# Performance work log

Measured on AMD Instinct MI355X. Metric: run time of the kernel, lower is better.

## Reference

```python
import jax, jax.numpy as jnp
import numpy as np

EPS = 1e-6


def _mlp(x, Ws, bs):
    # 5-layer MLP, exact (erf) GELU between layers, matching torch.nn.GELU()
    for W, b in zip(Ws[:-1], bs[:-1]):
        x = jax.nn.gelu(x @ W + b, approximate=False)
    return x @ Ws[-1] + bs[-1]


def setup_inputs() -> dict:
    key = jax.random.key(0)
    ks = jax.random.split(key, 16)
    B, H, D, NT = 262144, 256, 128, 16
    # deformation gradient near identity -> det(F) > 0 so log(det) is finite
    F = jnp.eye(3, dtype=jnp.float32)[None] + 0.05 * jax.random.normal(ks[0], (B, 3, 3), dtype=jnp.float32)
    C = 0.1 * jax.random.normal(ks[1], (B, 3, 3), dtype=jnp.float32)
    emb = 0.02 * jax.random.normal(ks[2], (NT, D), dtype=jnp.float32)
    dims = [16 + 9 + D, H, H, H, H, 9]
    inp = {"F": F, "C": C, "emb": emb, "traj_ids": 3}
    for i in range(5):
        inp[f"W{i+1}"] = jax.random.normal(ks[3 + 2 * i], (dims[i], dims[i + 1]), dtype=jnp.float32) / np.sqrt(dims[i]).astype(np.float32)
        inp[f"b{i+1}"] = jnp.zeros((dims[i + 1],), dtype=jnp.float32)
    return inp


def reference(F, C, emb, traj_ids, W1, b1, W2, b2, W3, b3, W4, b4, W5, b5):
    B = F.shape[0]
    U, sigma, Vh = jnp.linalg.svd(F)          # batched 3x3 SVD
    R = U @ Vh                                 # polar rotation, == torch U @ V^T
    Ft = jnp.swapaxes(F, -1, -2)
    FtF = Ft @ F
    det = jnp.linalg.det(F)
    f00 = jnp.maximum(F[:, 0, 0], EPS)
    # normalize_input=True branch: subtract 1 from each invariant
    I1 = sigma - 1.0                                   # [B,3]
    I2 = (FtF - jnp.eye(3, dtype=F.dtype)).reshape(B, 9)
    I3 = det[:, None] - 1.0
    I4 = jnp.log(det)[:, None] - 1.0
    I5 = f00[:, None] - 1.0
    I6 = jnp.log(f00)[:, None] - 1.0
    strain = jnp.concatenate([I1, I2, I3, I4, I5, I6], axis=1)  # [B,16]
    latent = jnp.broadcast_to(emb[traj_ids][None, :], (B, emb.shape[1]))
    feats = jnp.concatenate([strain, C.reshape(B, 9), latent], axis=-1)
    out = _mlp(feats, [W1, W2, W3, W4, W5], [b1, b2, b3, b4, b5])  # [B,9]
    x = out.reshape(B, 3, 3)
    x = 0.5 * (jnp.swapaxes(x, -1, -2) + x)    # symmetrize
    P = R @ x
    cauchy = P @ Ft
    return cauchy
```

## Files before the change

kernel.cpp:

```cpp
#include <hip/hip_runtime.h>

typedef _Float16 f16;
typedef _Float16 f16x8 __attribute__((ext_vector_type(8)));
typedef float f32x2 __attribute__((ext_vector_type(2)));
typedef float f32x4 __attribute__((ext_vector_type(4)));
typedef float f32x16 __attribute__((ext_vector_type(16)));

#define MROWS 128
#define THREADS 512
#define HSTR 264

#define WS_B1EFF 0
#define WS_W1H   1024
#define WS_W2H   (WS_W1H + 16384)
#define WS_W3H   (WS_W2H + 131072)
#define WS_W4H   (WS_W3H + 131072)
#define WS_W5H   (WS_W4H + 131072)
#define WS_END   (WS_W5H + 8192)

__global__ void prep_kernel(const float* __restrict__ emb, const int* __restrict__ traj,
                            const float* __restrict__ W1, const float* __restrict__ b1,
                            const float* __restrict__ W2, const float* __restrict__ W3,
                            const float* __restrict__ W4, const float* __restrict__ W5,
                            float* __restrict__ b1eff,
                            f16* __restrict__ W1h, f16* __restrict__ W2h,
                            f16* __restrict__ W3h, f16* __restrict__ W4h,
                            f16* __restrict__ W5h) {
  if (blockIdx.x == 816) {
    __shared__ float lat[128];
    int t = *traj;
    if (threadIdx.x < 128) lat[threadIdx.x] = emb[t * 128 + threadIdx.x];
    __syncthreads();
    int n = threadIdx.x;
    float s0 = 0.f, s1 = 0.f, s2 = 0.f, s3 = 0.f;
#pragma unroll 4
    for (int d = 0; d < 128; d += 4) {
      s0 = fmaf(lat[d + 0], W1[(25 + d) * 256 + n], s0);
      s1 = fmaf(lat[d + 1], W1[(26 + d) * 256 + n], s1);
      s2 = fmaf(lat[d + 2], W1[(27 + d) * 256 + n], s2);
      s3 = fmaf(lat[d + 3], W1[(28 + d) * 256 + n], s3);
    }
    b1eff[n] = b1[n] + ((s0 + s1) + (s2 + s3));
    return;
  }
  int i = blockIdx.x * 256 + threadIdx.x;
  if (i < 8192) {
    int n = i >> 5, k = i & 31;
    W1h[i] = (f16)((k < 25) ? W1[k * 256 + n] : 0.0f);
  } else if (i < 73728) {
    int j = i - 8192; int k = j >> 8, n = j & 255;
    W2h[n * 256 + k] = (f16)W2[j];
  } else if (i < 139264) {
    int j = i - 73728; int k = j >> 8, n = j & 255;
    W3h[n * 256 + k] = (f16)W3[j];
  } else if (i < 204800) {
    int j = i - 139264; int k = j >> 8, n = j & 255;
    W4h[n * 256 + k] = (f16)W4[j];
  } else if (i < 208896) {
    int j = i - 204800; int n = j >> 8, k = j & 255;
    W5h[j] = (f16)((n < 9) ? W5[k * 9 + n] : 0.0f);
  }
}

__device__ __forceinline__ f32x2 gelu2(f32x2 z) {
  f32x2 s = z * z;
  f32x2 q = __builtin_elementwise_fma(s, (f32x2)(-1.8889263e-5f), (f32x2)(2.30872094e-4f));
  q = __builtin_elementwise_fma(s, q, (f32x2)(-0.0023746714834f));
  q = __builtin_elementwise_fma(s, q, (f32x2)(0.01994711402007f));
  q = __builtin_elementwise_fma(s, q, (f32x2)(-0.13298076013381f));
  q = __builtin_elementwise_fma(s, q, (f32x2)(0.79788456080287f));
  f32x2 t = z * q;
  f32x2 u = 0.5f * z;
  return __builtin_elementwise_fma(u, t, u);
}

__global__ __launch_bounds__(THREADS, 4) void fused_kernel(
    const float* __restrict__ Fg, const float* __restrict__ Cg,
    const f16* __restrict__ W1h, const f16* __restrict__ W2h,
    const f16* __restrict__ W3h, const f16* __restrict__ W4h,
    const f16* __restrict__ W5h,
    const float* __restrict__ b1eff, const float* __restrict__ b2,
    const float* __restrict__ b3, const float* __restrict__ b4,
    const float* __restrict__ b5, float* __restrict__ outg, int Btot) {
  __shared__ __align__(16) f16 hA[MROWS * HSTR];
  __shared__ __align__(16) char uFO[MROWS * 64];
  __shared__ __align__(16) float sR[MROWS * 9];

  const int tid = threadIdx.x;
  const int lane = tid & 63;
  const int wv = tid >> 6;
  const int quad = lane >> 4;
  const int l15 = lane & 15;
  const int l31 = lane & 31;
  const int kh = lane >> 5;
  const int row0 = blockIdx.x * MROWS;

  if (tid < MROWS) {
    const int grow = row0 + tid;
    float feat[25];
    float Rm[9];
    if (grow < Btot) {
      float Fm[9], Cm[9];
      const float* fp = Fg + grow * 9;
      const float* cp = Cg + grow * 9;
#pragma unroll
      for (int i = 0; i < 9; ++i) Fm[i] = fp[i];
#pragma unroll
      for (int i = 0; i < 9; ++i) Cm[i] = cp[i];
      float G[9];
#pragma unroll
      for (int i = 0; i < 3; ++i)
#pragma unroll
        for (int j = 0; j < 3; ++j)
          G[i * 3 + j] = Fm[i] * Fm[j] + Fm[3 + i] * Fm[3 + j] + Fm[6 + i] * Fm[6 + j];
      float det = Fm[0] * (Fm[4] * Fm[8] - Fm[5] * Fm[7])
                - Fm[1] * (Fm[3] * Fm[8] - Fm[5] * Fm[6])
                + Fm[2] * (Fm[3] * Fm[7] - Fm[4] * Fm[6]);
#pragma unroll
      for (int i = 0; i < 9; ++i) Rm[i] = Fm[i];
#pragma unroll
      for (int it = 0; it < 5; ++it) {
        float c0 = Rm[4]*Rm[8] - Rm[5]*Rm[7];
        float c1 = Rm[5]*Rm[6] - Rm[3]*Rm[8];
        float c2 = Rm[3]*Rm[7] - Rm[4]*Rm[6];
        float c3 = Rm[2]*Rm[7] - Rm[1]*Rm[8];
        float c4 = Rm[0]*Rm[8] - Rm[2]*Rm[6];
        float c5 = Rm[1]*Rm[6] - Rm[0]*Rm[7];
        float c6 = Rm[1]*Rm[5] - Rm[2]*Rm[4];
        float c7 = Rm[2]*Rm[3] - Rm[0]*Rm[5];
        float c8 = Rm[0]*Rm[4] - Rm[1]*Rm[3];
        float dr = Rm[0]*c0 + Rm[1]*c1 + Rm[2]*c2;
        float hv = 0.5f / dr;
        Rm[0] = 0.5f*Rm[0] + hv*c0; Rm[1] = 0.5f*Rm[1] + hv*c1; Rm[2] = 0.5f*Rm[2] + hv*c2;
        Rm[3] = 0.5f*Rm[3] + hv*c3; Rm[4] = 0.5f*Rm[4] + hv*c4; Rm[5] = 0.5f*Rm[5] + hv*c5;
        Rm[6] = 0.5f*Rm[6] + hv*c6; Rm[7] = 0.5f*Rm[7] + hv*c7; Rm[8] = 0.5f*Rm[8] + hv*c8;
      }
      float s00 = Rm[0]*Fm[0] + Rm[3]*Fm[3] + Rm[6]*Fm[6];
      float s11 = Rm[1]*Fm[1] + Rm[4]*Fm[4] + Rm[7]*Fm[7];
      float s22 = Rm[2]*Fm[2] + Rm[5]*Fm[5] + Rm[8]*Fm[8];
      float s01 = 0.5f*((Rm[0]*Fm[1]+Rm[3]*Fm[4]+Rm[6]*Fm[7]) + (Rm[1]*Fm[0]+Rm[4]*Fm[3]+Rm[7]*Fm[6]));
      float s02 = 0.5f*((Rm[0]*Fm[2]+Rm[3]*Fm[5]+Rm[6]*Fm[8]) + (Rm[2]*Fm[0]+Rm[5]*Fm[3]+Rm[8]*Fm[6]));
      float s12 = 0.5f*((Rm[1]*Fm[2]+Rm[4]*Fm[5]+Rm[7]*Fm[8]) + (Rm[2]*Fm[1]+Rm[5]*Fm[4]+Rm[8]*Fm[7]));
      float q  = (s00 + s11 + s22) * (1.0f/3.0f);
      float p1 = s01*s01 + s02*s02 + s12*s12;
      float d0 = s00 - q, d1 = s11 - q, d2 = s22 - q;
      float p2 = d0*d0 + d1*d1 + d2*d2 + 2.0f*p1;
      float p  = sqrtf(p2 * (1.0f/6.0f));
      float e1, e2, e3;
      if (p > 1e-10f) {
        float pi = 1.0f / p;
        float b00 = d0*pi, b11 = d1*pi, b22 = d2*pi;
        float b01 = s01*pi, b02 = s02*pi, b12 = s12*pi;
        float detB = b00*(b11*b22 - b12*b12) - b01*(b01*b22 - b12*b02) + b02*(b01*b12 - b11*b02);
        float r = fminf(fmaxf(0.5f*detB, -1.0f), 1.0f);
        float phi = acosf(r) * (1.0f/3.0f);
        e1 = q + 2.0f * p * cosf(phi);
        e3 = q + 2.0f * p * cosf(phi + 2.0943951023931953f);
        e2 = 3.0f*q - e1 - e3;
      } else { e1 = q; e2 = q; e3 = q; }
      float f00 = fmaxf(Fm[0], 1e-6f);
      feat[0] = e1 - 1.0f; feat[1] = e2 - 1.0f; feat[2] = e3 - 1.0f;
#pragma unroll
      for (int k = 0; k < 9; ++k) feat[3 + k] = G[k];
      feat[3] -= 1.0f; feat[7] -= 1.0f; feat[11] -= 1.0f;
      feat[12] = det - 1.0f;
      feat[13] = logf(det) - 1.0f;
      feat[14] = f00 - 1.0f;
      feat[15] = logf(f00) - 1.0f;
#pragma unroll
      for (int k = 0; k < 9; ++k) feat[16 + k] = Cm[k];
    } else {
#pragma unroll
      for (int k = 0; k < 25; ++k) feat[k] = 0.0f;
#pragma unroll
      for (int k = 0; k < 9; ++k) Rm[k] = 0.0f;
    }
#pragma unroll
    for (int k = 0; k < 9; ++k) sR[tid * 9 + k] = Rm[k];
#pragma unroll
    for (int c = 0; c < 4; ++c) {
      f16x8 v;
#pragma unroll
      for (int j = 0; j < 8; ++j) {
        int k = c * 8 + j;
        v[j] = (f16)((k < 25) ? feat[k] : 0.0f);
      }
      *(f16x8*)(uFO + tid * 64 + c * 16) = v;
    }
  }
  __syncthreads();

  {
#pragma unroll
    for (int t = 0; t < 2; ++t) {
      const int col = wv * 32 + t * 16 + l15;
      f16x8 bfr = *(const f16x8*)(W1h + col * 32 + quad * 8);
      float bias = b1eff[col];
#pragma unroll
      for (int st = 0; st < 8; ++st) {
        const int arow = st * 16 + l15;
        f16x8 a = *(const f16x8*)(uFO + arow * 64 + quad * 16);
        f32x4 acc = (f32x4){bias, bias, bias, bias};
        acc = __builtin_amdgcn_mfma_f32_16x16x32_f16(a, bfr, acc, 0, 0, 0);
        f32x2 g0 = gelu2((f32x2){acc[0], acc[1]});
        f32x2 g1 = gelu2((f32x2){acc[2], acc[3]});
        const int orow = st * 16 + quad * 4;
        hA[(orow + 0) * HSTR + col] = (f16)g0[0];
        hA[(orow + 1) * HSTR + col] = (f16)g0[1];
        hA[(orow + 2) * HSTR + col] = (f16)g1[0];
        hA[(orow + 3) * HSTR + col] = (f16)g1[1];
      }
    }
  }
  __syncthreads();

  const f16* Whs[3] = {W2h, W3h, W4h};
  const float* bgs[3] = {b2, b3, b4};
  const int col32 = wv * 32 + l31;
#pragma unroll 1
  for (int L = 0; L < 3; ++L) {
    const f16* Wh = Whs[L];
    const float bias = bgs[L][col32];
    f32x16 acc0, acc1, acc2, acc3;
#pragma unroll
    for (int r = 0; r < 16; ++r) { acc0[r] = bias; acc1[r] = bias; acc2[r] = bias; acc3[r] = bias; }
#pragma unroll
    for (int q = 0; q < 4; ++q) {
      f16x8 bq[4];
#pragma unroll
      for (int j = 0; j < 4; ++j)
        bq[j] = *(const f16x8*)(Wh + col32 * 256 + (q * 4 + j) * 16 + kh * 8);
#pragma unroll
      for (int j = 0; j < 4; ++j) {
        f16x8 a = *(const f16x8*)(hA + l31 * HSTR + (q * 4 + j) * 16 + kh * 8);
        acc0 = __builtin_amdgcn_mfma_f32_32x32x16_f16(a, bq[j], acc0, 0, 0, 0);
      }
#pragma unroll
      for (int j = 0; j < 4; ++j) {
        f16x8 a = *(const f16x8*)(hA + (32 + l31) * HSTR + (q * 4 + j) * 16 + kh * 8);
        acc1 = __builtin_amdgcn_mfma_f32_32x32x16_f16(a, bq[j], acc1, 0, 0, 0);
      }
#pragma unroll
      for (int j = 0; j < 4; ++j) {
        f16x8 a = *(const f16x8*)(hA + (64 + l31) * HSTR + (q * 4 + j) * 16 + kh * 8);
        acc2 = __builtin_amdgcn_mfma_f32_32x32x16_f16(a, bq[j], acc2, 0, 0, 0);
      }
#pragma unroll
      for (int j = 0; j < 4; ++j) {
        f16x8 a = *(const f16x8*)(hA + (96 + l31) * HSTR + (q * 4 + j) * 16 + kh * 8);
        acc3 = __builtin_amdgcn_mfma_f32_32x32x16_f16(a, bq[j], acc3, 0, 0, 0);
      }
    }
    f16 hv0[16], hv1[16], hv2[16], hv3[16];
#pragma unroll
    for (int r2 = 0; r2 < 8; ++r2) {
      f32x2 g0 = gelu2((f32x2){acc0[2 * r2], acc0[2 * r2 + 1]});
      f32x2 g1 = gelu2((f32x2){acc1[2 * r2], acc1[2 * r2 + 1]});
      f32x2 g2 = gelu2((f32x2){acc2[2 * r2], acc2[2 * r2 + 1]});
      f32x2 g3 = gelu2((f32x2){acc3[2 * r2], acc3[2 * r2 + 1]});
      hv0[2 * r2] = (f16)g0[0]; hv0[2 * r2 + 1] = (f16)g0[1];
      hv1[2 * r2] = (f16)g1[0]; hv1[2 * r2 + 1] = (f16)g1[1];
      hv2[2 * r2] = (f16)g2[0]; hv2[2 * r2 + 1] = (f16)g2[1];
      hv3[2 * r2] = (f16)g3[0]; hv3[2 * r2 + 1] = (f16)g3[1];
    }
    __syncthreads();
#pragma unroll
    for (int r = 0; r < 16; ++r) {
      const int orow = (r & 3) + 8 * (r >> 2) + 4 * kh;
      hA[orow * HSTR + col32]        = hv0[r];
      hA[(32 + orow) * HSTR + col32] = hv1[r];
      hA[(64 + orow) * HSTR + col32] = hv2[r];
      hA[(96 + orow) * HSTR + col32] = hv3[r];
    }
    __syncthreads();
  }

  {
    float* o32 = (float*)uFO;
    f16x8 bf5[8];
#pragma unroll
    for (int s = 0; s < 8; ++s)
      bf5[s] = *(const f16x8*)(W5h + l15 * 256 + s * 32 + quad * 8);
    const int arow = wv * 16 + l15;
    float bv = (l15 < 9) ? b5[l15] : 0.0f;
    f32x4 acc = (f32x4){bv, bv, bv, bv};
#pragma unroll
    for (int s = 0; s < 8; ++s) {
      f16x8 a = *(const f16x8*)(hA + arow * HSTR + s * 32 + quad * 8);
      acc = __builtin_amdgcn_mfma_f32_16x16x32_f16(a, bf5[s], acc, 0, 0, 0);
    }
#pragma unroll
    for (int r = 0; r < 4; ++r) {
      const int orow = wv * 16 + quad * 4 + r;
      o32[orow * 16 + l15] = acc[r];
    }
  }
  __syncthreads();

  float* stage = (float*)hA;
  const float* o32c = (const float*)uFO;
  if (tid < MROWS && row0 + tid < Btot) {
    const float* x = o32c + tid * 16;
    const float* fp = Fg + (row0 + tid) * 9;
    float Fm[9], Rm[9];
#pragma unroll
    for (int i = 0; i < 9; ++i) Fm[i] = fp[i];
#pragma unroll
    for (int i = 0; i < 9; ++i) Rm[i] = sR[tid * 9 + i];
    float y[9];
    y[0] = x[0]; y[4] = x[4]; y[8] = x[8];
    y[1] = 0.5f * (x[1] + x[3]); y[3] = y[1];
    y[2] = 0.5f * (x[2] + x[6]); y[6] = y[2];
    y[5] = 0.5f * (x[5] + x[7]); y[7] = y[5];
    float P[9];
#pragma unroll
    for (int i = 0; i < 3; ++i)
#pragma unroll
      for (int j = 0; j < 3; ++j)
        P[i*3+j] = Rm[i*3]*y[j] + Rm[i*3+1]*y[3+j] + Rm[i*3+2]*y[6+j];
#pragma unroll
    for (int i = 0; i < 3; ++i)
#pragma unroll
      for (int j = 0; j < 3; ++j)
        stage[tid*9 + i*3 + j] = P[i*3]*Fm[j*3] + P[i*3+1]*Fm[j*3+1] + P[i*3+2]*Fm[j*3+2];
  }
  __syncthreads();
  for (int i = tid; i < MROWS * 9; i += THREADS) {
    int gi = row0 * 9 + i;
    if (gi < Btot * 9) outg[gi] = stage[i];
  }
}

extern "C" void kernel_launch(void* const* d_in, const int* in_sizes, int n_in,
                              void* d_out, int out_size, void* d_ws, size_t ws_size,
                              hipStream_t stream) {
  const float* Fg  = (const float*)d_in[0];
  const float* Cg  = (const float*)d_in[1];
  const float* emb = (const float*)d_in[2];
  const int*   trj = (const int*)d_in[3];
  const float* W1  = (const float*)d_in[4];
  const float* b1  = (const float*)d_in[5];
  const float* W2  = (const float*)d_in[6];
  const float* b2  = (const float*)d_in[7];
  const float* W3  = (const float*)d_in[8];
  const float* b3  = (const float*)d_in[9];
  const float* W4  = (const float*)d_in[10];
  const float* b4  = (const float*)d_in[11];
  const float* W5  = (const float*)d_in[12];
  const float* b5  = (const float*)d_in[13];
  float* outg = (float*)d_out;
  const int Btot = in_sizes[0] / 9;

  char* ws = (char*)d_ws;
  float* b1eff = (float*)(ws + WS_B1EFF);
  f16* W1h = (f16*)(ws + WS_W1H);
  f16* W2h = (f16*)(ws + WS_W2H);
  f16* W3h = (f16*)(ws + WS_W3H);
  f16* W4h = (f16*)(ws + WS_W4H);
  f16* W5h = (f16*)(ws + WS_W5H);

  prep_kernel<<<817, 256, 0, stream>>>(emb, trj, W1, b1, W2, W3, W4, W5,
                                       b1eff, W1h, W2h, W3h, W4h, W5h);
  const int grid = (Btot + MROWS - 1) / MROWS;
  fused_kernel<<<grid, THREADS, 0, stream>>>(Fg, Cg, W1h, W2h, W3h, W4h, W5h,
                                             b1eff, b2, b3, b4, b5, outg, Btot);
}
```

Before: 264.4 us.

## Keep MLP activations in registers and stage swizzled weights in LDS

Restructures the fused MLP so each wave owns 32 rows and carries its activations in registers across all layers. The transposed MFMA output is reshaped into the next layer's operand with cross-half lane shuffles instead of round-tripping through LDS. Each hidden-layer weight matrix (128KB fp16) is staged into LDS with an XOR swizzle to avoid bank conflicts, and biases are pre-permuted into accumulator order. Block size grows to 256 rows, occupancy drops to 2 blocks per CU, and a full weight reload per layer with barriers stalls all waves.

Result: slower. 342.0 us (+29.3%).

```diff
diff --git a/kernel.cpp b/kernel.cpp
--- a/kernel.cpp
+++ b/kernel.cpp
@@ -5,29 +5,34 @@
 typedef float f32x2 __attribute__((ext_vector_type(2)));
 typedef float f32x4 __attribute__((ext_vector_type(4)));
 typedef float f32x16 __attribute__((ext_vector_type(16)));
-
-#define MROWS 128
+typedef unsigned int u32;
+typedef unsigned int u32x4 __attribute__((ext_vector_type(4)));
+
 #define THREADS 512
-#define HSTR 264
+#define BROWS 256
 
 #define WS_B1EFF 0
-#define WS_W1H   1024
-#define WS_W2H   (WS_W1H + 16384)
+#define WS_BPERM 1024
+#define WS_W1H   6144
+#define WS_W2H   22528
 #define WS_W3H   (WS_W2H + 131072)
 #define WS_W4H   (WS_W3H + 131072)
 #define WS_W5H   (WS_W4H + 131072)
-#define WS_END   (WS_W5H + 8192)
+#define WS_END   (WS_W5H + 16384)
 
 __global__ void prep_kernel(const float* __restrict__ emb, const int* __restrict__ traj,
                             const float* __restrict__ W1, const float* __restrict__ b1,
-                            const float* __restrict__ W2, const float* __restrict__ W3,
-                            const float* __restrict__ W4, const float* __restrict__ W5,
-                            float* __restrict__ b1eff,
+                            const float* __restrict__ W2, const float* __restrict__ b2,
+                            const float* __restrict__ W3, const float* __restrict__ b3,
+                            const float* __restrict__ W4, const float* __restrict__ b4,
+                            const float* __restrict__ W5, const float* __restrict__ b5,
+                            float* __restrict__ b1eff, float* __restrict__ bperm,
                             f16* __restrict__ W1h, f16* __restrict__ W2h,
                             f16* __restrict__ W3h, f16* __restrict__ W4h,
                             f16* __restrict__ W5h) {
-  if (blockIdx.x == 816) {
+  if (blockIdx.x == 832) {
     __shared__ float lat[128];
+    __shared__ float bsh[256];
     int t = *traj;
     if (threadIdx.x < 128) lat[threadIdx.x] = emb[t * 128 + threadIdx.x];
     __syncthreads();
@@ -40,7 +45,17 @@
       s2 = fmaf(lat[d + 2], W1[(27 + d) * 256 + n], s2);
       s3 = fmaf(lat[d + 3], W1[(28 + d) * 256 + n], s3);
     }
-    b1eff[n] = b1[n] + ((s0 + s1) + (s2 + s3));
+    float v = b1[n] + ((s0 + s1) + (s2 + s3));
+    b1eff[n] = v; bsh[n] = v;
+    __syncthreads();
+    int i = threadIdx.x;
+    int nt = i >> 5, khh = (i >> 4) & 1, r = i & 15;
+    int nn = 32 * nt + (r & 3) + 8 * (r >> 2) + 4 * khh;
+    bperm[0 * 256 + i] = bsh[nn];
+    bperm[1 * 256 + i] = b2[nn];
+    bperm[2 * 256 + i] = b3[nn];
+    bperm[3 * 256 + i] = b4[nn];
+    bperm[4 * 256 + i] = (nn < 9) ? b5[nn] : 0.0f;
     return;
   }
   int i = blockIdx.x * 256 + threadIdx.x;
@@ -49,14 +64,14 @@
     W1h[i] = (f16)((k < 25) ? W1[k * 256 + n] : 0.0f);
   } else if (i < 73728) {
     int j = i - 8192; int k = j >> 8, n = j & 255;
-    W2h[n * 256 + k] = (f16)W2[j];
+    W2h[(n * 256 + k) ^ ((n & 7) << 3)] = (f16)W2[j];
   } else if (i < 139264) {
     int j = i - 73728; int k = j >> 8, n = j & 255;
-    W3h[n * 256 + k] = (f16)W3[j];
+    W3h[(n * 256 + k) ^ ((n & 7) << 3)] = (f16)W3[j];
   } else if (i < 204800) {
     int j = i - 139264; int k = j >> 8, n = j & 255;
-    W4h[n * 256 + k] = (f16)W4[j];
-  } else if (i < 208896) {
+    W4h[(n * 256 + k) ^ ((n & 7) << 3)] = (f16)W4[j];
+  } else if (i < 212992) {
     int j = i - 204800; int n = j >> 8, k = j & 255;
     W5h[j] = (f16)((n < 9) ? W5[k * 9 + n] : 0.0f);
   }
@@ -74,239 +89,231 @@
   return __builtin_elementwise_fma(u, t, u);
 }
 
-__global__ __launch_bounds__(THREADS, 4) void fused_kernel(
+__device__ __forceinline__ u32 pack2(float a, float b) {
+  unsigned short ha = __builtin_bit_cast(unsigned short, (f16)a);
+  unsigned short hb = __builtin_bit_cast(unsigned short, (f16)b);
+  return (u32)ha | ((u32)hb << 16);
+}
+
+__device__ __forceinline__ void exch_pack(const f32x16 acc, int kh, f16x8* fa, f16x8* fb) {
+  float g[16];
+#pragma unroll
+  for (int i = 0; i < 8; ++i) {
+    f32x2 r = gelu2((f32x2){acc[2 * i], acc[2 * i + 1]});
+    g[2 * i] = r[0]; g[2 * i + 1] = r[1];
+  }
+  u32 P[8];
+#pragma unroll
+  for (int i = 0; i < 8; ++i) P[i] = pack2(g[2 * i], g[2 * i + 1]);
+  u32 s[8];
+#pragma unroll
+  for (int i = 0; i < 8; ++i) s[i] = (u32)__shfl_xor((int)P[i], 32);
+  u32x4 ua, ub;
+  ua[0] = kh ? s[2] : P[0];
+  ua[1] = kh ? s[3] : P[1];
+  ua[2] = kh ? P[2] : s[0];
+  ua[3] = kh ? P[3] : s[1];
+  ub[0] = kh ? s[6] : P[4];
+  ub[1] = kh ? s[7] : P[5];
+  ub[2] = kh ? P[6] : s[4];
+  ub[3] = kh ? P[7] : s[5];
+  *fa = __builtin_bit_cast(f16x8, ua);
+  *fb = __builtin_bit_cast(f16x8, ub);
+}
+
+__device__ __forceinline__ void stage_w(const f16* __restrict__ src, f16* dst, int tid) {
+#pragma unroll
+  for (int rdi = 0; rdi < 4; ++rdi) {
+    f16x8 t0 = *(const f16x8*)(src + (rdi * 4 + 0) * 4096 + tid * 8);
+    f16x8 t1 = *(const f16x8*)(src + (rdi * 4 + 1) * 4096 + tid * 8);
+    f16x8 t2 = *(const f16x8*)(src + (rdi * 4 + 2) * 4096 + tid * 8);
+    f16x8 t3 = *(const f16x8*)(src + (rdi * 4 + 3) * 4096 + tid * 8);
+    *(f16x8*)(dst + (rdi * 4 + 0) * 4096 + tid * 8) = t0;
+    *(f16x8*)(dst + (rdi * 4 + 1) * 4096 + tid * 8) = t1;
+    *(f16x8*)(dst + (rdi * 4 + 2) * 4096 + tid * 8) = t2;
+    *(f16x8*)(dst + (rdi * 4 + 3) * 4096 + tid * 8) = t3;
+  }
+}
+
+__global__ __launch_bounds__(THREADS, 2) void fused_kernel(
     const float* __restrict__ Fg, const float* __restrict__ Cg,
     const f16* __restrict__ W1h, const f16* __restrict__ W2h,
     const f16* __restrict__ W3h, const f16* __restrict__ W4h,
-    const f16* __restrict__ W5h,
-    const float* __restrict__ b1eff, const float* __restrict__ b2,
-    const float* __restrict__ b3, const float* __restrict__ b4,
-    const float* __restrict__ b5, float* __restrict__ outg, int Btot) {
-  __shared__ __align__(16) f16 hA[MROWS * HSTR];
-  __shared__ __align__(16) char uFO[MROWS * 64];
-  __shared__ __align__(16) float sR[MROWS * 9];
+    const f16* __restrict__ W5h, const float* __restrict__ bperm,
+    float* __restrict__ outg, int Btot) {
+  __shared__ __align__(16) f16 Wlds[65536];
 
   const int tid = threadIdx.x;
   const int lane = tid & 63;
   const int wv = tid >> 6;
-  const int quad = lane >> 4;
-  const int l15 = lane & 15;
   const int l31 = lane & 31;
   const int kh = lane >> 5;
-  const int row0 = blockIdx.x * MROWS;
-
-  if (tid < MROWS) {
-    const int grow = row0 + tid;
-    float feat[25];
-    float Rm[9];
-    if (grow < Btot) {
-      float Fm[9], Cm[9];
-      const float* fp = Fg + grow * 9;
-      const float* cp = Cg + grow * 9;
-#pragma unroll
-      for (int i = 0; i < 9; ++i) Fm[i] = fp[i];
-#pragma unroll
-      for (int i = 0; i < 9; ++i) Cm[i] = cp[i];
-      float G[9];
-#pragma unroll
-      for (int i = 0; i < 3; ++i)
-#pragma unroll
-        for (int j = 0; j < 3; ++j)
-          G[i * 3 + j] = Fm[i] * Fm[j] + Fm[3 + i] * Fm[3 + j] + Fm[6 + i] * Fm[6 + j];
-      float det = Fm[0] * (Fm[4] * Fm[8] - Fm[5] * Fm[7])
-                - Fm[1] * (Fm[3] * Fm[8] - Fm[5] * Fm[6])
-                + Fm[2] * (Fm[3] * Fm[7] - Fm[4] * Fm[6]);
-#pragma unroll
-      for (int i = 0; i < 9; ++i) Rm[i] = Fm[i];
-#pragma unroll
-      for (int it = 0; it < 5; ++it) {
-        float c0 = Rm[4]*Rm[8] - Rm[5]*Rm[7];
-        float c1 = Rm[5]*Rm[6] - Rm[3]*Rm[8];
-        float c2 = Rm[3]*Rm[7] - Rm[4]*Rm[6];
-        float c3 = Rm[2]*Rm[7] - Rm[1]*Rm[8];
-        float c4 = Rm[0]*Rm[8] - Rm[2]*Rm[6];
-        float c5 = Rm[1]*Rm[6] - Rm[0]*Rm[7];
-        float c6 = Rm[1]*Rm[5] - Rm[2]*Rm[4];
-        float c7 = Rm[2]*Rm[3] - Rm[0]*Rm[5];
-        float c8 = Rm[0]*Rm[4] - Rm[1]*Rm[3];
-        float dr = Rm[0]*c0 + Rm[1]*c1 + Rm[2]*c2;
-        float hv = 0.5f / dr;
-        Rm[0] = 0.5f*Rm[0] + hv*c0; Rm[1] = 0.5f*Rm[1] + hv*c1; Rm[2] = 0.5f*Rm[2] + hv*c2;
-        Rm[3] = 0.5f*Rm[3] + hv*c3; Rm[4] = 0.5f*Rm[4] + hv*c4; Rm[5] = 0.5f*Rm[5] + hv*c5;
-        Rm[6] = 0.5f*Rm[6] + hv*c6; Rm[7] = 0.5f*Rm[7] + hv*c7; Rm[8] = 0.5f*Rm[8] + hv*c8;
-      }
-      float s00 = Rm[0]*Fm[0] + Rm[3]*Fm[3] + Rm[6]*Fm[6];
-      float s11 = Rm[1]*Fm[1] + Rm[4]*Fm[4] + Rm[7]*Fm[7];
-      float s22 = Rm[2]*Fm[2] + Rm[5]*Fm[5] + Rm[8]*Fm[8];
-      float s01 = 0.5f*((Rm[0]*Fm[1]+Rm[3]*Fm[4]+Rm[6]*Fm[7]) + (Rm[1]*Fm[0]+Rm[4]*Fm[3]+Rm[7]*Fm[6]));
-      float s02 = 0.5f*((Rm[0]*Fm[2]+Rm[3]*Fm[5]+Rm[6]*Fm[8]) + (Rm[2]*Fm[0]+Rm[5]*Fm[3]+Rm[8]*Fm[6]));
-      float s12 = 0.5f*((Rm[1]*Fm[2]+Rm[4]*Fm[5]+Rm[7]*Fm[8]) + (Rm[2]*Fm[1]+Rm[5]*Fm[4]+Rm[8]*Fm[7]));
-      float q  = (s00 + s11 + s22) * (1.0f/3.0f);
-      float p1 = s01*s01 + s02*s02 + s12*s12;
-      float d0 = s00 - q, d1 = s11 - q, d2 = s22 - q;
-      float p2 = d0*d0 + d1*d1 + d2*d2 + 2.0f*p1;
-      float p  = sqrtf(p2 * (1.0f/6.0f));
-      float e1, e2, e3;
-      if (p > 1e-10f) {
-        float pi = 1.0f / p;
-        float b00 = d0*pi, b11 = d1*pi, b22 = d2*pi;
-        float b01 = s01*pi, b02 = s02*pi, b12 = s12*pi;
-        float detB = b00*(b11*b22 - b12*b12) - b01*(b01*b22 - b12*b02) + b02*(b01*b12 - b11*b02);
-        float r = fminf(fmaxf(0.5f*detB, -1.0f), 1.0f);
-        float phi = acosf(r) * (1.0f/3.0f);
-        e1 = q + 2.0f * p * cosf(phi);
-        e3 = q + 2.0f * p * cosf(phi + 2.0943951023931953f);
-        e2 = 3.0f*q - e1 - e3;
-      } else { e1 = q; e2 = q; e3 = q; }
-      float f00 = fmaxf(Fm[0], 1e-6f);
-      feat[0] = e1 - 1.0f; feat[1] = e2 - 1.0f; feat[2] = e3 - 1.0f;
-#pragma unroll
-      for (int k = 0; k < 9; ++k) feat[3 + k] = G[k];
-      feat[3] -= 1.0f; feat[7] -= 1.0f; feat[11] -= 1.0f;
-      feat[12] = det - 1.0f;
-      feat[13] = logf(det) - 1.0f;
-      feat[14] = f00 - 1.0f;
-      feat[15] = logf(f00) - 1.0f;
-#pragma unroll
-      for (int k = 0; k < 9; ++k) feat[16 + k] = Cm[k];
-    } else {
-#pragma unroll
-      for (int k = 0; k < 25; ++k) feat[k] = 0.0f;
-#pragma unroll
-      for (int k = 0; k < 9; ++k) Rm[k] = 0.0f;
-    }
-#pragma unroll
-    for (int k = 0; k < 9; ++k) sR[tid * 9 + k] = Rm[k];
-#pragma unroll
-    for (int c = 0; c < 4; ++c) {
-      f16x8 v;
-#pragma unroll
-      for (int j = 0; j < 8; ++j) {
-        int k = c * 8 + j;
-        v[j] = (f16)((k < 25) ? feat[k] : 0.0f);
-      }
-      *(f16x8*)(uFO + tid * 64 + c * 16) = v;
-    }
-  }
-  __syncthreads();
-
+  const int myrow = blockIdx.x * BROWS + wv * 32 + l31;
+
+  stage_w(W2h, Wlds, tid);
+
+  float feat[25];
+  float Rm[9];
+  if (myrow < Btot) {
+    float Fm[9], Cm[9];
+    const float* fp = Fg + myrow * 9;
+    const float* cp = Cg + myrow * 9;
+#pragma unroll
+    for (int i = 0; i < 9; ++i) Fm[i] = fp[i];
+#pragma unroll
+    for (int i = 0; i < 9; ++i) Cm[i] = cp[i];
+    float G[9];
+#pragma unroll
+    for (int i = 0; i < 3; ++i)
+#pragma unroll
+      for (int j = 0; j < 3; ++j)
+        G[i * 3 + j] = Fm[i] * Fm[j] + Fm[3 + i] * Fm[3 + j] + Fm[6 + i] * Fm[6 + j];
+    float det = Fm[0] * (Fm[4] * Fm[8] - Fm[5] * Fm[7])
+              - Fm[1] * (Fm[3] * Fm[8] - Fm[5] * Fm[6])
+              + Fm[2] * (Fm[3] * Fm[7] - Fm[4] * Fm[6]);
+#pragma unroll
+    for (int i = 0; i < 9; ++i) Rm[i] = Fm[i];
+#pragma unroll
+    for (int it = 0; it < 5; ++it) {
+      float c0 = Rm[4]*Rm[8] - Rm[5]*Rm[7];
+      float c1 = Rm[5]*Rm[6] - Rm[3]*Rm[8];
+      float c2 = Rm[3]*Rm[7] - Rm[4]*Rm[6];
+      float c3 = Rm[2]*Rm[7] - Rm[1]*Rm[8];
+      float c4 = Rm[0]*Rm[8] - Rm[2]*Rm[6];
+      float c5 = Rm[1]*Rm[6] - Rm[0]*Rm[7];
+      float c6 = Rm[1]*Rm[5] - Rm[2]*Rm[4];
+      float c7 = Rm[2]*Rm[3] - Rm[0]*Rm[5];
+      float c8 = Rm[0]*Rm[4] - Rm[1]*Rm[3];
+      float dr = Rm[0]*c0 + Rm[1]*c1 + Rm[2]*c2;
+      float hv = 0.5f / dr;
+      Rm[0] = 0.5f*Rm[0] + hv*c0; Rm[1] = 0.5f*Rm[1] + hv*c1; Rm[2] = 0.5f*Rm[2] + hv*c2;
+      Rm[3] = 0.5f*Rm[3] + hv*c3; Rm[4] = 0.5f*Rm[4] + hv*c4; Rm[5] = 0.5f*Rm[5] + hv*c5;
+      Rm[6] = 0.5f*Rm[6] + hv*c6; Rm[7] = 0.5f*Rm[7] + hv*c7; Rm[8] = 0.5f*Rm[8] + hv*c8;
+    }
+    float s00 = Rm[0]*Fm[0] + Rm[3]*Fm[3] + Rm[6]*Fm[6];
+    float s11 = Rm[1]*Fm[1] + Rm[4]*Fm[4] + Rm[7]*Fm[7];
+    float s22 = Rm[2]*Fm[2] + Rm[5]*Fm[5] + Rm[8]*Fm[8];
+    float s01 = 0.5f*((Rm[0]*Fm[1]+Rm[3]*Fm[4]+Rm[6]*Fm[7]) + (Rm[1]*Fm[0]+Rm[4]*Fm[3]+Rm[7]*Fm[6]));
+    float s02 = 0.5f*((Rm[0]*Fm[2]+Rm[3]*Fm[5]+Rm[6]*Fm[8]) + (Rm[2]*Fm[0]+Rm[5]*Fm[3]+Rm[8]*Fm[6]));
+    float s12 = 0.5f*((Rm[1]*Fm[2]+Rm[4]*Fm[5]+Rm[7]*Fm[8]) + (Rm[2]*Fm[1]+Rm[5]*Fm[4]+Rm[8]*Fm[7]));
+    float q  = (s00 + s11 + s22) * (1.0f/3.0f);
+    float p1 = s01*s01 + s02*s02 + s12*s12;
+    float d0 = s00 - q, d1 = s11 - q, d2 = s22 - q;
+    float p2 = d0*d0 + d1*d1 + d2*d2 + 2.0f*p1;
+    float p  = sqrtf(p2 * (1.0f/6.0f));
+    float e1, e2, e3;
+    if (p > 1e-10f) {
+      float pi = 1.0f / p;
+      float b00 = d0*pi, b11 = d1*pi, b22 = d2*pi;
+      float b01 = s01*pi, b02 = s02*pi, b12 = s12*pi;
+      float detB = b00*(b11*b22 - b12*b12) - b01*(b01*b22 - b12*b02) + b02*(b01*b12 - b11*b02);
+      float r = fminf(fmaxf(0.5f*detB, -1.0f), 1.0f);
+      float phi = acosf(r) * (1.0f/3.0f);
+      e1 = q + 2.0f * p * cosf(phi);
+      e3 = q + 2.0f * p * cosf(phi + 2.0943951023931953f);
+      e2 = 3.0f*q - e1 - e3;
+    } else { e1 = q; e2 = q; e3 = q; }
+    float f00 = fmaxf(Fm[0], 1e-6f);
+    feat[0] = e1 - 1.0f; feat[1] = e2 - 1.0f; feat[2] = e3 - 1.0f;
+#pragma unroll
+    for (int k = 0; k < 9; ++k) feat[3 + k] = G[k];
+    feat[3] -= 1.0f; feat[7] -= 1.0f; feat[11] -= 1.0f;
+    feat[12] = det - 1.0f;
+    feat[13] = logf(det) - 1.0f;
+    feat[14] = f00 - 1.0f;
+    feat[15] = logf(f00) - 1.0f;
+#pragma unroll
+    for (int k = 0; k < 9; ++k) feat[16 + k] = Cm[k];
+  } else {
+#pragma unroll
+    for (int k = 0; k < 25; ++k) feat[k] = 0.0f;
+#pragma unroll
+    for (int k = 0; k < 9; ++k) Rm[k] = 0.0f;
+  }
+
+  f16x8 xa, xb;
+#pragma unroll
+  for (int j = 0; j < 8; ++j) xa[j] = (f16)(kh ? feat[8 + j] : feat[j]);
+#pragma unroll
+  for (int j = 0; j < 8; ++j) {
+    int k = 16 + 8 * kh + j;
+    xb[j] = (f16)((k < 25) ? feat[k] : 0.0f);
+  }
+
+  f16x8 X[16];
   {
-#pragma unroll
-    for (int t = 0; t < 2; ++t) {
-      const int col = wv * 32 + t * 16 + l15;
-      f16x8 bfr = *(const f16x8*)(W1h + col * 32 + quad * 8);
-      float bias = b1eff[col];
-#pragma unroll
-      for (int st = 0; st < 8; ++st) {
-        const int arow = st * 16 + l15;
-        f16x8 a = *(const f16x8*)(uFO + arow * 64 + quad * 16);
-        f32x4 acc = (f32x4){bias, bias, bias, bias};
-        acc = __builtin_amdgcn_mfma_f32_16x16x32_f16(a, bfr, acc, 0, 0, 0);
-        f32x2 g0 = gelu2((f32x2){acc[0], acc[1]});
-        f32x2 g1 = gelu2((f32x2){acc[2], acc[3]});
-        const int orow = st * 16 + quad * 4;
-        hA[(orow + 0) * HSTR + col] = (f16)g0[0];
-        hA[(orow + 1) * HSTR + col] = (f16)g0[1];
-        hA[(orow + 2) * HSTR + col] = (f16)g1[0];
-        hA[(orow + 3) * HSTR + col] = (f16)g1[1];
-      }
-    }
-  }
-  __syncthreads();
-
-  const f16* Whs[3] = {W2h, W3h, W4h};
-  const float* bgs[3] = {b2, b3, b4};
-  const int col32 = wv * 32 + l31;
+    const float* bp = bperm + 0 * 256 + kh * 16;
+#pragma unroll
+    for (int nt = 0; nt < 8; ++nt) {
+      const f32x4* bq = (const f32x4*)(bp + nt * 32);
+      f32x4 c0 = bq[0], c1 = bq[1], c2 = bq[2], c3 = bq[3];
+      f32x16 acc;
+#pragma unroll
+      for (int r = 0; r < 4; ++r) { acc[r] = c0[r]; acc[4 + r] = c1[r]; acc[8 + r] = c2[r]; acc[12 + r] = c3[r]; }
+      const f16* wb = W1h + (nt * 32 + l31) * 32 + kh * 8;
+      f16x8 w0 = *(const f16x8*)(wb);
+      f16x8 w1 = *(const f16x8*)(wb + 16);
+      acc = __builtin_amdgcn_mfma_f32_32x32x16_f16(w0, xa, acc, 0, 0, 0);
+      acc = __builtin_amdgcn_mfma_f32_32x32x16_f16(w1, xb, acc, 0, 0, 0);
+      exch_pack(acc, kh, &X[2 * nt], &X[2 * nt + 1]);
+    }
+  }
+
 #pragma unroll 1
   for (int L = 0; L < 3; ++L) {
-    const f16* Wh = Whs[L];
-    const float bias = bgs[L][col32];
-    f32x16 acc0, acc1, acc2, acc3;
-#pragma unroll
-    for (int r = 0; r < 16; ++r) { acc0[r] = bias; acc1[r] = bias; acc2[r] = bias; acc3[r] = bias; }
-#pragma unroll
-    for (int q = 0; q < 4; ++q) {
-      f16x8 bq[4];
-#pragma unroll
-      for (int j = 0; j < 4; ++j)
-        bq[j] = *(const f16x8*)(Wh + col32 * 256 + (q * 4 + j) * 16 + kh * 8);
-#pragma unroll
-      for (int j = 0; j < 4; ++j) {
-        f16x8 a = *(const f16x8*)(hA + l31 * HSTR + (q * 4 + j) * 16 + kh * 8);
-        acc0 = __builtin_amdgcn_mfma_f32_32x32x16_f16(a, bq[j], acc0, 0, 0, 0);
+    if (L > 0) {
+      __syncthreads();
+      stage_w((L == 1) ? W3h : W4h, Wlds, tid);
+    }
+    __syncthreads();
+    const float* bp = bperm + (L + 1) * 256 + kh * 16;
+    f16x8 Xn[16];
+#pragma unroll
+    for (int nt = 0; nt < 8; ++nt) {
+      const f32x4* bq = (const f32x4*)(bp + nt * 32);
+      f32x4 c0 = bq[0], c1 = bq[1], c2 = bq[2], c3 = bq[3];
+      f32x16 acc;
+#pragma unroll
+      for (int r = 0; r < 4; ++r) { acc[r] = c0[r]; acc[4 + r] = c1[r]; acc[8 + r] = c2[r]; acc[12 + r] = c3[r]; }
+#pragma unroll
+      for (int kt = 0; kt < 16; ++kt) {
+        const int a = ((nt * 32 + l31) * 256 + kt * 16 + kh * 8) ^ ((l31 & 7) << 3);
+        f16x8 w = *(const f16x8*)(Wlds + a);
+        acc = __builtin_amdgcn_mfma_f32_32x32x16_f16(w, X[kt], acc, 0, 0, 0);
       }
-#pragma unroll
-      for (int j = 0; j < 4; ++j) {
-        f16x8 a = *(const f16x8*)(hA + (32 + l31) * HSTR + (q * 4 + j) * 16 + kh * 8);
-        acc1 = __builtin_amdgcn_mfma_f32_32x32x16_f16(a, bq[j], acc1, 0, 0, 0);
-      }
-#pragma unroll
-      for (int j = 0; j < 4; ++j) {
-        f16x8 a = *(const f16x8*)(hA + (64 + l31) * HSTR + (q * 4 + j) * 16 + kh * 8);
-        acc2 = __builtin_amdgcn_mfma_f32_32x32x16_f16(a, bq[j], acc2, 0, 0, 0);
-      }
-#pragma unroll
-      for (int j = 0; j < 4; ++j) {
-        f16x8 a = *(const f16x8*)(hA + (96 + l31) * HSTR + (q * 4 + j) * 16 + kh * 8);
-        acc3 = __builtin_amdgcn_mfma_f32_32x32x16_f16(a, bq[j], acc3, 0, 0, 0);
-      }
-    }
-    f16 hv0[16], hv1[16], hv2[16], hv3[16];
-#pragma unroll
-    for (int r2 = 0; r2 < 8; ++r2) {
-      f32x2 g0 = gelu2((f32x2){acc0[2 * r2], acc0[2 * r2 + 1]});
-      f32x2 g1 = gelu2((f32x2){acc1[2 * r2], acc1[2 * r2 + 1]});
-      f32x2 g2 = gelu2((f32x2){acc2[2 * r2], acc2[2 * r2 + 1]});
-      f32x2 g3 = gelu2((f32x2){acc3[2 * r2], acc3[2 * r2 + 1]});
-      hv0[2 * r2] = (f16)g0[0]; hv0[2 * r2 + 1] = (f16)g0[1];
-      hv1[2 * r2] = (f16)g1[0]; hv1[2 * r2 + 1] = (f16)g1[1];
-      hv2[2 * r2] = (f16)g2[0]; hv2[2 * r2 + 1] = (f16)g2[1];
-      hv3[2 * r2] = (f16)g3[0]; hv3[2 * r2 + 1] = (f16)g3[1];
-    }
-    __syncthreads();
-#pragma unroll
-    for (int r = 0; r < 16; ++r) {
-      const int orow = (r & 3) + 8 * (r >> 2) + 4 * kh;
-      hA[orow * HSTR + col32]        = hv0[r];
-      hA[(32 + orow) * HSTR + col32] = hv1[r];
-      hA[(64 + orow) * HSTR + col32] = hv2[r];
-      hA[(96 + orow) * HSTR + col32] = hv3[r];
-    }
-    __syncthreads();
-  }
-
+      exch_pack(acc, kh, &Xn[2 * nt], &Xn[2 * nt + 1]);
+    }
+#pragma unroll
+    for (int t2 = 0; t2 < 16; ++t2) X[t2] = Xn[t2];
+  }
+
+  f32x16 acc5;
   {
-    float* o32 = (float*)uFO;
-    f16x8 bf5[8];
-#pragma unroll
-    for (int s = 0; s < 8; ++s)
-      bf5[s] = *(const f16x8*)(W5h + l15 * 256 + s * 32 + quad * 8);
-    const int arow = wv * 16 + l15;
-    float bv = (l15 < 9) ? b5[l15] : 0.0f;
-    f32x4 acc = (f32x4){bv, bv, bv, bv};
-#pragma unroll
-    for (int s = 0; s < 8; ++s) {
-      f16x8 a = *(const f16x8*)(hA + arow * HSTR + s * 32 + quad * 8);
-      acc = __builtin_amdgcn_mfma_f32_16x16x32_f16(a, bf5[s], acc, 0, 0, 0);
-    }
-#pragma unroll
-    for (int r = 0; r < 4; ++r) {
-      const int orow = wv * 16 + quad * 4 + r;
-      o32[orow * 16 + l15] = acc[r];
-    }
-  }
-  __syncthreads();
-
-  float* stage = (float*)hA;
-  const float* o32c = (const float*)uFO;
-  if (tid < MROWS && row0 + tid < Btot) {
-    const float* x = o32c + tid * 16;
-    const float* fp = Fg + (row0 + tid) * 9;
-    float Fm[9], Rm[9];
+    const float* bp = bperm + 4 * 256 + kh * 16;
+    const f32x4* bq = (const f32x4*)(bp);
+    f32x4 c0 = bq[0], c1 = bq[1], c2 = bq[2], c3 = bq[3];
+#pragma unroll
+    for (int r = 0; r < 4; ++r) { acc5[r] = c0[r]; acc5[4 + r] = c1[r]; acc5[8 + r] = c2[r]; acc5[12 + r] = c3[r]; }
+#pragma unroll
+    for (int kt = 0; kt < 16; ++kt) {
+      f16x8 w = *(const f16x8*)(W5h + l31 * 256 + kt * 16 + kh * 8);
+      acc5 = __builtin_amdgcn_mfma_f32_32x32x16_f16(w, X[kt], acc5, 0, 0, 0);
+    }
+  }
+
+  float sx0 = __shfl_xor(acc5[0], 32);
+  float sx1 = __shfl_xor(acc5[1], 32);
+  float sx2 = __shfl_xor(acc5[2], 32);
+  float sx3 = __shfl_xor(acc5[3], 32);
+  if (kh == 0 && myrow < Btot) {
+    float x[9];
+    x[0] = acc5[0]; x[1] = acc5[1]; x[2] = acc5[2]; x[3] = acc5[3];
+    x[4] = sx0; x[5] = sx1; x[6] = sx2; x[7] = sx3;
+    x[8] = acc5[4];
+    const float* fp = Fg + myrow * 9;
+    float Fm[9];
 #pragma unroll
     for (int i = 0; i < 9; ++i) Fm[i] = fp[i];
-#pragma unroll
-    for (int i = 0; i < 9; ++i) Rm[i] = sR[tid * 9 + i];
     float y[9];
     y[0] = x[0]; y[4] = x[4]; y[8] = x[8];
     y[1] = 0.5f * (x[1] + x[3]); y[3] = y[1];
@@ -322,12 +329,7 @@
     for (int i = 0; i < 3; ++i)
 #pragma unroll
       for (int j = 0; j < 3; ++j)
-        stage[tid*9 + i*3 + j] = P[i*3]*Fm[j*3] + P[i*3+1]*Fm[j*3+1] + P[i*3+2]*Fm[j*3+2];
-  }
-  __syncthreads();
-  for (int i = tid; i < MROWS * 9; i += THREADS) {
-    int gi = row0 * 9 + i;
-    if (gi < Btot * 9) outg[gi] = stage[i];
+        outg[myrow * 9 + i*3 + j] = P[i*3]*Fm[j*3] + P[i*3+1]*Fm[j*3+1] + P[i*3+2]*Fm[j*3+2];
   }
 }
 
@@ -353,15 +355,17 @@
 
   char* ws = (char*)d_ws;
   float* b1eff = (float*)(ws + WS_B1EFF);
+  float* bperm = (float*)(ws + WS_BPERM);
   f16* W1h = (f16*)(ws + WS_W1H);
   f16* W2h = (f16*)(ws + WS_W2H);
   f16* W3h = (f16*)(ws + WS_W3H);
   f16* W4h = (f16*)(ws + WS_W4H);
   f16* W5h = (f16*)(ws + WS_W5H);
 
-  prep_kernel<<<817, 256, 0, stream>>>(emb, trj, W1, b1, W2, W3, W4, W5,
-                                       b1eff, W1h, W2h, W3h, W4h, W5h);
-  const int grid = (Btot + MROWS - 1) / MROWS;
+  prep_kernel<<<833, 256, 0, stream>>>(emb, trj, W1, b1, W2, b2, W3, b3, W4, b4,
+                                       W5, b5, b1eff, bperm,
+                                       W1h, W2h, W3h, W4h, W5h);
+  const int grid = (Btot + BROWS - 1) / BROWS;
   fused_kernel<<<grid, THREADS, 0, stream>>>(Fg, Cg, W1h, W2h, W3h, W4h, W5h,
-                                             b1eff, b2, b3, b4, b5, outg, Btot);
-}
+                                             bperm, outg, Btot);
+}
```
